# Optimization experiments

Measured on AMD Instinct MI355X. Metric: run time of the kernel, lower is better.

The kernel has to match this reference:

```python
import jax, jax.numpy as jnp
import numpy as np


def setup_inputs() -> dict:
    key = jax.random.key(0)
    k1, k2 = jax.random.split(key)
    n_nodes, d_feat, n_edges = 100000, 48, 1600000
    x = jax.random.normal(k1, (n_nodes, d_feat), dtype=jnp.float32)
    edge_index = jax.random.randint(k2, (2, n_edges), 0, n_nodes, dtype=jnp.int64)
    return {"x": x, "edge_index": edge_index, "batch_size": 65536}


def reference(x, edge_index, batch_size):
    # adj = SparseTensor.from_edge_index(edge_index): adj[row, col] = 1 with
    # row = edge_index[0] (src), col = edge_index[1] (dst).
    # adj.t() @ x  ->  out[i] = sum over edges (src -> i) of x[src]
    src, dst = edge_index[0], edge_index[1]
    n_nodes = x.shape[0]
    # memory-bound gather + scatter-add (SpMM, sum aggregation)
    x_neighbors_sum = jax.ops.segment_sum(x[src], dst, num_segments=n_nodes)
    node_labels = jnp.concatenate(
        (x[:batch_size, :], x_neighbors_sum[:batch_size, :]), axis=-1
    )
    return node_labels
```

## Files before the change

### kernel.cpp

```cpp
#include <hip/hip_runtime.h>
#include <hip/hip_fp16.h>

#define DFEAT 48
#define OUTW  96
#define NBINB 512
#define BINTH 512
#define EPT   7
#define NBUCK2 512
#define RBITS 7
#define NROWS 128
#define RAWCAP 2560
#define CSRCAP 2560


static __device__ __forceinline__ unsigned short f2h(float f) {
    __half h = __float2half_rn(f);
    return *reinterpret_cast<unsigned short*>(&h);
}

static __device__ __forceinline__ int wave_iscan(int v, int lane) {
    #pragma unroll
    for (int d = 1; d < 64; d <<= 1) {
        int tv = __shfl_up(v, d, 64);
        if (lane >= d) v += tv;
    }
    return v;
}

__global__ __launch_bounds__(BINTH)
void bin_k(const int* __restrict__ ei, int n_edges, int batch, int chunk,
           const float4* __restrict__ x4, int nx4, uint2* __restrict__ xh4,
           unsigned short* __restrict__ starts, unsigned int* __restrict__ regions,
           int use_half) {
    __shared__ int cnt[NBUCK2];
    __shared__ int cur[NBUCK2];
    __shared__ int wsum[BINTH / 64];
    __shared__ int totS;
    const int t = threadIdx.x;
    const int b = blockIdx.x;
    const int lane = t & 63, wid = t >> 6;

    if (use_half) {
        for (int i = b * BINTH + t; i < nx4; i += NBINB * BINTH) {
            float4 v = x4[i];
            xh4[i] = make_uint2((unsigned)f2h(v.x) | ((unsigned)f2h(v.y) << 16),
                                (unsigned)f2h(v.z) | ((unsigned)f2h(v.w) << 16));
        }
    }

    const int beg = b * chunk;
    const int end = min(beg + chunk, n_edges);

    unsigned int pay[EPT];
    int bkt[EPT];
    #pragma unroll
    for (int i = 0; i < EPT; i++) {
        bkt[i] = -1;
        int e = beg + t + i * BINTH;
        if (e < end) {
            int dst = ei[n_edges + e];
            if (dst < batch) {
                int src = ei[e];
                bkt[i] = dst >> RBITS;
                pay[i] = ((unsigned)(dst & (NROWS - 1)) << 17) | (unsigned)src;
            }
        }
    }
    cnt[t] = 0;
    __syncthreads();
    #pragma unroll
    for (int i = 0; i < EPT; i++)
        if (bkt[i] >= 0) atomicAdd(&cnt[bkt[i]], 1);
    __syncthreads();
    int v = cnt[t];
    int iv = wave_iscan(v, lane);
    if (lane == 63) wsum[wid] = iv;
    __syncthreads();
    if (t < BINTH / 64) {
        int wv = wsum[t];
        int sv = wave_iscan(wv, t);
        wsum[t] = sv - wv;
        if (t == BINTH / 64 - 1) totS = sv;
    }
    __syncthreads();
    int excl = iv - v + wsum[wid];
    cur[t] = excl;
    starts[t * NBINB + b] = (unsigned short)excl;
    if (t == 0) starts[NBUCK2 * NBINB + b] = (unsigned short)totS;
    __syncthreads();
    unsigned int* reg = regions + (size_t)b * chunk;
    #pragma unroll
    for (int i = 0; i < EPT; i++)
        if (bkt[i] >= 0) {
            int pos = atomicAdd(&cur[bkt[i]], 1);
            reg[pos] = pay[i];
        }
}

__global__ __launch_bounds__(1024)
void reduce_k(const float* __restrict__ x, const uint2* __restrict__ xh2,
              const unsigned short* __restrict__ starts,
              const unsigned int* __restrict__ regions,
              float* __restrict__ out, int batch, int chunk, int use_half) {
    __shared__ unsigned int raw[RAWCAP];
    __shared__ int csr[CSRCAP];
    __shared__ int cnt[NROWS], off[NROWS + 1], cur[NROWS];
    __shared__ int wsum[16];
    __shared__ int totS;
    const int t = threadIdx.x;
    const int kb = blockIdx.x;
    const int lane = t & 63, wid = t >> 6;

    int s0 = 0, len = 0;
    if (t < NBINB) {
        s0 = starts[kb * NBINB + t];
        int s1 = starts[(kb + 1) * NBINB + t];
        len = s1 - s0;
    }
    int iv = wave_iscan(len, lane);
    if (lane == 63 && wid < 8) wsum[wid] = iv;
    __syncthreads();
    if (t < 8) {
        int wv = wsum[t];
        int sv = wave_iscan(wv, t);
        wsum[t] = sv - wv;
        if (t == 7) totS = sv;
    }
    __syncthreads();
    const int T = min(totS, RAWCAP);
    if (t < NBINB && len > 0) {
        int base = iv - len + wsum[wid];
        const unsigned int* reg = regions + (size_t)t * chunk + s0;
        if (len <= 8) {
            #pragma unroll
            for (int i = 0; i < 8; i++) {
                if (i < len) {
                    int p = base + i;
                    if (p < RAWCAP) raw[p] = reg[i];
                }
            }
        } else {
            for (int i = 0; i < len; i++) {
                int p = base + i;
                if (p < RAWCAP) raw[p] = reg[i];
            }
        }
    }
    if (t < NROWS) cnt[t] = 0;
    __syncthreads();
    for (int i = t; i < T; i += 1024) atomicAdd(&cnt[raw[i] >> 17], 1);
    __syncthreads();
    int v2 = (t < NROWS) ? cnt[t] : 0;
    int iv2 = wave_iscan(v2, lane);
    if (lane == 63 && wid < 2) wsum[wid] = iv2;
    __syncthreads();
    if (t == 0) {
        int a = wsum[0];
        off[NROWS] = a + wsum[1];
        wsum[1] = a;
        wsum[0] = 0;
    }
    __syncthreads();
    if (t < NROWS) {
        int excl = iv2 - v2 + wsum[wid];
        off[t] = excl;
        cur[t] = excl;
    }
    __syncthreads();
    for (int i = t; i < T; i += 1024) {
        unsigned int p = raw[i];
        int pos = atomicAdd(&cur[p >> 17], 1);
        if (pos < CSRCAP) csr[pos] = (int)(p & 0x1FFFFu);
    }
    __syncthreads();

    if (use_half) {
        const int g  = lane / 12;
        const int cg = lane - g * 12;
        const bool act = lane < 48;
        const float4* x4 = (const float4*)x;
        float4* out4 = (float4*)out;
        #pragma unroll
        for (int rr = 0; rr < 4; rr++) {
            const int ra = wid + 16 * rr;
            const int rb = ra + 64;
            const int rowA = kb * NROWS + ra;
            const int rowB = kb * NROWS + rb;
            const bool okA = rowA < batch, okB = rowB < batch;
            int e0a = 0, e1a = 0, e0b = 0, e1b = 0;
            if (okA) { e0a = off[ra]; e1a = min(off[ra + 1], CSRCAP); }
            if (okB) { e0b = off[rb]; e1b = min(off[rb + 1], CSRCAP); }
            float4 accA = make_float4(0.f, 0.f, 0.f, 0.f);
            float4 accB = make_float4(0.f, 0.f, 0.f, 0.f);
            int na = e1a - e0a, nb2 = e1b - e0b;
            int n = na > nb2 ? na : nb2;
            for (int k = 0; k < n; k += 8) {
                if (act) {
                    int a1 = e0a + k + g, a2 = e0a + k + 4 + g;
                    int b1 = e0b + k + g, b2 = e0b + k + 4 + g;
                    if (a1 < e1a) {
                        uint2 p = xh2[(size_t)csr[a1] * 12 + cg];
                        float2 f0 = __half22float2(*(const __half2*)&p.x);
                        float2 f1 = __half22float2(*(const __half2*)&p.y);
                        accA.x += f0.x; accA.y += f0.y; accA.z += f1.x; accA.w += f1.y;
                    }
                    if (b1 < e1b) {
                        uint2 p = xh2[(size_t)csr[b1] * 12 + cg];
                        float2 f0 = __half22float2(*(const __half2*)&p.x);
                        float2 f1 = __half22float2(*(const __half2*)&p.y);
                        accB.x += f0.x; accB.y += f0.y; accB.z += f1.x; accB.w += f1.y;
                    }
                    if (a2 < e1a) {
                        uint2 p = xh2[(size_t)csr[a2] * 12 + cg];
                        float2 f0 = __half22float2(*(const __half2*)&p.x);
                        float2 f1 = __half22float2(*(const __half2*)&p.y);
                        accA.x += f0.x; accA.y += f0.y; accA.z += f1.x; accA.w += f1.y;
                    }
                    if (b2 < e1b) {
                        uint2 p = xh2[(size_t)csr[b2] * 12 + cg];
                        float2 f0 = __half22float2(*(const __half2*)&p.x);
                        float2 f1 = __half22float2(*(const __half2*)&p.y);
                        accB.x += f0.x; accB.y += f0.y; accB.z += f1.x; accB.w += f1.y;
                    }
                }
            }
            float4 bb;
            bb.x = __shfl(accA.x, lane + 24); bb.y = __shfl(accA.y, lane + 24);
            bb.z = __shfl(accA.z, lane + 24); bb.w = __shfl(accA.w, lane + 24);
            if (lane < 24) { accA.x += bb.x; accA.y += bb.y; accA.z += bb.z; accA.w += bb.w; }
            bb.x = __shfl(accA.x, lane + 12); bb.y = __shfl(accA.y, lane + 12);
            bb.z = __shfl(accA.z, lane + 12); bb.w = __shfl(accA.w, lane + 12);
            if (lane < 12 && okA) {
                accA.x += bb.x; accA.y += bb.y; accA.z += bb.z; accA.w += bb.w;
                out4[(size_t)rowA * 24 + 12 + cg] = accA;
                out4[(size_t)rowA * 24 + cg] = x4[(size_t)rowA * 12 + cg];
            }
            bb.x = __shfl(accB.x, lane + 24); bb.y = __shfl(accB.y, lane + 24);
            bb.z = __shfl(accB.z, lane + 24); bb.w = __shfl(accB.w, lane + 24);
            if (lane < 24) { accB.x += bb.x; accB.y += bb.y; accB.z += bb.z; accB.w += bb.w; }
            bb.x = __shfl(accB.x, lane + 12); bb.y = __shfl(accB.y, lane + 12);
            bb.z = __shfl(accB.z, lane + 12); bb.w = __shfl(accB.w, lane + 12);
            if (lane < 12 && okB) {
                accB.x += bb.x; accB.y += bb.y; accB.z += bb.z; accB.w += bb.w;
                out4[(size_t)rowB * 24 + 12 + cg] = accB;
                out4[(size_t)rowB * 24 + cg] = x4[(size_t)rowB * 12 + cg];
            }
        }
    } else {
        if (lane < DFEAT) {
            for (int r = wid; r < NROWS; r += 16) {
                int row = kb * NROWS + r;
                if (row >= batch) break;
                int e0 = off[r], e1 = min(off[r + 1], CSRCAP);
                float acc = 0.f;
                for (int e = e0; e < e1; ++e)
                    acc += x[(size_t)csr[e] * DFEAT + lane];
                out[(size_t)row * OUTW + lane]         = x[(size_t)row * DFEAT + lane];
                out[(size_t)row * OUTW + DFEAT + lane] = acc;
            }
        }
    }
}


#define D4   12
#define ROW4 24

__global__ void init_out_kernel(const float4* __restrict__ x4,
                                float4* __restrict__ out4, int batch) {
    int idx = blockIdx.x * blockDim.x + threadIdx.x;
    int total = batch * ROW4;
    if (idx >= total) return;
    int row = idx / ROW4;
    int c   = idx - row * ROW4;
    float4 v;
    if (c < D4) v = x4[row * D4 + c];
    else        v = make_float4(0.f, 0.f, 0.f, 0.f);
    out4[idx] = v;
}

__global__ void scatter_edges_kernel(const float4* __restrict__ x4,
                                     const int* __restrict__ ei,
                                     float* __restrict__ out,
                                     int n_edges, int batch) {
    int tid = blockIdx.x * blockDim.x + threadIdx.x;
    int e = tid / D4;
    int q = tid - e * D4;
    if (e >= n_edges) return;
    int dst = ei[n_edges + e];
    if (dst >= batch) return;
    int src = ei[e];
    float4 v = x4[src * D4 + q];
    float* p = out + (size_t)dst * OUTW + DFEAT + q * 4;
    atomicAdd(p + 0, v.x);
    atomicAdd(p + 1, v.y);
    atomicAdd(p + 2, v.z);
    atomicAdd(p + 3, v.w);
}


extern "C" void kernel_launch(void* const* d_in, const int* in_sizes, int n_in,
                              void* d_out, int out_size, void* d_ws, size_t ws_size,
                              hipStream_t stream) {
    const float* x  = (const float*)d_in[0];
    const int*   ei = (const int*)d_in[1];
    float* out = (float*)d_out;

    const int n_edges = in_sizes[1] / 2;
    const int batch   = out_size / OUTW;
    const int n_nodes = in_sizes[0] / DFEAT;
    const int chunk   = (n_edges + NBINB - 1) / NBINB;
    const int nbuck   = (batch + NROWS - 1) / NROWS;
    const int nx4     = n_nodes * DFEAT / 4;

    size_t xh_bytes = ((size_t)n_nodes * DFEAT * sizeof(unsigned short) + 15) & ~(size_t)15;
    size_t starts_bytes = (size_t)(NBUCK2 + 1) * NBINB * sizeof(unsigned short);
    size_t reg_bytes = (size_t)NBINB * chunk * sizeof(unsigned int);
    size_t need_h = xh_bytes + starts_bytes + reg_bytes;
    size_t need_f = starts_bytes + reg_bytes;

    bool base_ok = chunk <= BINTH * EPT && chunk < 65536 &&
                   n_nodes <= (1 << 17) && batch <= NBUCK2 * NROWS &&
                   (n_nodes * DFEAT) % 4 == 0 && nbuck >= 1 && nbuck <= NBUCK2;

    if (base_ok && ws_size >= need_h) {
        unsigned short* xh = (unsigned short*)d_ws;
        unsigned short* starts = (unsigned short*)((char*)d_ws + xh_bytes);
        unsigned int* regions = (unsigned int*)((char*)d_ws + xh_bytes + starts_bytes);
        bin_k<<<NBINB, BINTH, 0, stream>>>(ei, n_edges, batch, chunk,
                                           (const float4*)x, nx4, (uint2*)xh,
                                           starts, regions, 1);
        reduce_k<<<nbuck, 1024, 0, stream>>>(x, (const uint2*)xh, starts, regions,
                                             out, batch, chunk, 1);
    } else if (base_ok && ws_size >= need_f) {
        unsigned short* starts = (unsigned short*)d_ws;
        unsigned int* regions = (unsigned int*)((char*)d_ws + starts_bytes);
        bin_k<<<NBINB, BINTH, 0, stream>>>(ei, n_edges, batch, chunk,
                                           (const float4*)x, nx4, (uint2*)0,
                                           starts, regions, 0);
        reduce_k<<<nbuck, 1024, 0, stream>>>(x, (const uint2*)0, starts, regions,
                                             out, batch, chunk, 0);
    } else {
        {
            int total = batch * ROW4;
            int grid = (total + 255) / 256;
            init_out_kernel<<<grid, 256, 0, stream>>>((const float4*)x,
                                                      (float4*)out, batch);
        }
        {
            long long total = (long long)n_edges * D4;
            long long grid = (total + 255) / 256;
            scatter_edges_kernel<<<(int)grid, 256, 0, stream>>>(
                (const float4*)x, ei, out, n_edges, batch);
        }
    }
}
```

Before: 126.1 us.

## Stage binned edges in LDS, move x-copy into bin pass, prescale CSR indices

The bin kernel now scatters edge payloads into a shared-memory sorted buffer and writes them to global memory in one contiguous, coalesced pass, replacing scattered global writes. It also copies the first half of each output row (x itself) while converting x to half precision, so the reduce kernel no longer re-reads x for that purpose. CSR entries are premultiplied by 12 to save an index multiply in the gather loop. The fp32 fallback path now indexes x with csr*4, which matches the prescaled index, but in that path the x-copy in bin_k never runs, though reduce_k still writes it. The added SORTCAP limit of 3584 and the batch%128 requirement narrow when the fast path is used.

```diff
diff --git a/kernel.cpp b/kernel.cpp
--- a/kernel.cpp
+++ b/kernel.cpp
@@ -6,6 +6,7 @@
 #define NBINB 512
 #define BINTH 512
 #define EPT   7
+#define SORTCAP 3584
 #define NBUCK2 512
 #define RBITS 7
 #define NROWS 128
@@ -31,20 +32,26 @@
 void bin_k(const int* __restrict__ ei, int n_edges, int batch, int chunk,
            const float4* __restrict__ x4, int nx4, uint2* __restrict__ xh4,
            unsigned short* __restrict__ starts, unsigned int* __restrict__ regions,
-           int use_half) {
+           float4* __restrict__ out4, int use_half) {
     __shared__ int cnt[NBUCK2];
     __shared__ int cur[NBUCK2];
     __shared__ int wsum[BINTH / 64];
     __shared__ int totS;
+    __shared__ unsigned int sorted[SORTCAP];
     const int t = threadIdx.x;
     const int b = blockIdx.x;
     const int lane = t & 63, wid = t >> 6;
 
     if (use_half) {
+        const int batch12 = batch * 12;
         for (int i = b * BINTH + t; i < nx4; i += NBINB * BINTH) {
             float4 v = x4[i];
             xh4[i] = make_uint2((unsigned)f2h(v.x) | ((unsigned)f2h(v.y) << 16),
                                 (unsigned)f2h(v.z) | ((unsigned)f2h(v.w) << 16));
+            if (i < batch12) {
+                int row = i / 12, cg = i - row * 12;
+                out4[(size_t)row * 24 + cg] = v;
+            }
         }
     }
 
@@ -84,17 +91,20 @@
     }
     __syncthreads();
     int excl = iv - v + wsum[wid];
+    int tot = totS;
     cur[t] = excl;
     starts[t * NBINB + b] = (unsigned short)excl;
-    if (t == 0) starts[NBUCK2 * NBINB + b] = (unsigned short)totS;
-    __syncthreads();
-    unsigned int* reg = regions + (size_t)b * chunk;
+    if (t == 0) starts[NBUCK2 * NBINB + b] = (unsigned short)tot;
+    __syncthreads();
     #pragma unroll
     for (int i = 0; i < EPT; i++)
         if (bkt[i] >= 0) {
             int pos = atomicAdd(&cur[bkt[i]], 1);
-            reg[pos] = pay[i];
-        }
+            sorted[pos] = pay[i];
+        }
+    __syncthreads();
+    unsigned int* reg = regions + (size_t)b * chunk;
+    for (int i = t; i < tot; i += BINTH) reg[i] = sorted[i];
 }
 
 __global__ __launch_bounds__(1024)
@@ -170,7 +180,7 @@
     for (int i = t; i < T; i += 1024) {
         unsigned int p = raw[i];
         int pos = atomicAdd(&cur[p >> 17], 1);
-        if (pos < CSRCAP) csr[pos] = (int)(p & 0x1FFFFu);
+        if (pos < CSRCAP) csr[pos] = (int)(p & 0x1FFFFu) * 12;
     }
     __syncthreads();
 
@@ -178,7 +188,6 @@
         const int g  = lane / 12;
         const int cg = lane - g * 12;
         const bool act = lane < 48;
-        const float4* x4 = (const float4*)x;
         float4* out4 = (float4*)out;
         #pragma unroll
         for (int rr = 0; rr < 4; rr++) {
@@ -199,25 +208,25 @@
                     int a1 = e0a + k + g, a2 = e0a + k + 4 + g;
                     int b1 = e0b + k + g, b2 = e0b + k + 4 + g;
                     if (a1 < e1a) {
-                        uint2 p = xh2[(size_t)csr[a1] * 12 + cg];
+                        uint2 p = xh2[(size_t)csr[a1] + cg];
                         float2 f0 = __half22float2(*(const __half2*)&p.x);
                         float2 f1 = __half22float2(*(const __half2*)&p.y);
                         accA.x += f0.x; accA.y += f0.y; accA.z += f1.x; accA.w += f1.y;
                     }
                     if (b1 < e1b) {
-                        uint2 p = xh2[(size_t)csr[b1] * 12 + cg];
+                        uint2 p = xh2[(size_t)csr[b1] + cg];
                         float2 f0 = __half22float2(*(const __half2*)&p.x);
                         float2 f1 = __half22float2(*(const __half2*)&p.y);
                         accB.x += f0.x; accB.y += f0.y; accB.z += f1.x; accB.w += f1.y;
                     }
                     if (a2 < e1a) {
-                        uint2 p = xh2[(size_t)csr[a2] * 12 + cg];
+                        uint2 p = xh2[(size_t)csr[a2] + cg];
                         float2 f0 = __half22float2(*(const __half2*)&p.x);
                         float2 f1 = __half22float2(*(const __half2*)&p.y);
                         accA.x += f0.x; accA.y += f0.y; accA.z += f1.x; accA.w += f1.y;
                     }
                     if (b2 < e1b) {
-                        uint2 p = xh2[(size_t)csr[b2] * 12 + cg];
+                        uint2 p = xh2[(size_t)csr[b2] + cg];
                         float2 f0 = __half22float2(*(const __half2*)&p.x);
                         float2 f1 = __half22float2(*(const __half2*)&p.y);
                         accB.x += f0.x; accB.y += f0.y; accB.z += f1.x; accB.w += f1.y;
@@ -233,7 +242,6 @@
             if (lane < 12 && okA) {
                 accA.x += bb.x; accA.y += bb.y; accA.z += bb.z; accA.w += bb.w;
                 out4[(size_t)rowA * 24 + 12 + cg] = accA;
-                out4[(size_t)rowA * 24 + cg] = x4[(size_t)rowA * 12 + cg];
             }
             bb.x = __shfl(accB.x, lane + 24); bb.y = __shfl(accB.y, lane + 24);
             bb.z = __shfl(accB.z, lane + 24); bb.w = __shfl(accB.w, lane + 24);
@@ -243,7 +251,6 @@
             if (lane < 12 && okB) {
                 accB.x += bb.x; accB.y += bb.y; accB.z += bb.z; accB.w += bb.w;
                 out4[(size_t)rowB * 24 + 12 + cg] = accB;
-                out4[(size_t)rowB * 24 + cg] = x4[(size_t)rowB * 12 + cg];
             }
         }
     } else {
@@ -254,7 +261,7 @@
                 int e0 = off[r], e1 = min(off[r + 1], CSRCAP);
                 float acc = 0.f;
                 for (int e = e0; e < e1; ++e)
-                    acc += x[(size_t)csr[e] * DFEAT + lane];
+                    acc += x[(size_t)csr[e] * 4 + lane];
                 out[(size_t)row * OUTW + lane]         = x[(size_t)row * DFEAT + lane];
                 out[(size_t)row * OUTW + DFEAT + lane] = acc;
             }
@@ -319,9 +326,10 @@
     size_t need_h = xh_bytes + starts_bytes + reg_bytes;
     size_t need_f = starts_bytes + reg_bytes;
 
-    bool base_ok = chunk <= BINTH * EPT && chunk < 65536 &&
+    bool base_ok = chunk <= SORTCAP && chunk <= BINTH * EPT && chunk < 65536 &&
                    n_nodes <= (1 << 17) && batch <= NBUCK2 * NROWS &&
-                   (n_nodes * DFEAT) % 4 == 0 && nbuck >= 1 && nbuck <= NBUCK2;
+                   (n_nodes * DFEAT) % 4 == 0 && nbuck >= 1 && nbuck <= NBUCK2 &&
+                   batch % NROWS == 0;
 
     if (base_ok && ws_size >= need_h) {
         unsigned short* xh = (unsigned short*)d_ws;
@@ -329,7 +337,7 @@
         unsigned int* regions = (unsigned int*)((char*)d_ws + xh_bytes + starts_bytes);
         bin_k<<<NBINB, BINTH, 0, stream>>>(ei, n_edges, batch, chunk,
                                            (const float4*)x, nx4, (uint2*)xh,
-                                           starts, regions, 1);
+                                           starts, regions, (float4*)out, 1);
         reduce_k<<<nbuck, 1024, 0, stream>>>(x, (const uint2*)xh, starts, regions,
                                              out, batch, chunk, 1);
     } else if (base_ok && ws_size >= need_f) {
@@ -337,7 +345,7 @@
         unsigned int* regions = (unsigned int*)((char*)d_ws + starts_bytes);
         bin_k<<<NBINB, BINTH, 0, stream>>>(ei, n_edges, batch, chunk,
                                            (const float4*)x, nx4, (uint2*)0,
-                                           starts, regions, 0);
+                                           starts, regions, (float4*)out, 0);
         reduce_k<<<nbuck, 1024, 0, stream>>>(x, (const uint2*)0, starts, regions,
                                              out, batch, chunk, 0);
     } else {
```

Measured after the change: 121.3 us. -3.8%, faster.
